# Performance work log

Hardware: AMD Instinct MI355X
Metric: run time of the kernel (lower is better)

The kernel has to match this reference:

```python
import jax, jax.numpy as jnp
import numpy as np

P, B, A, NBT, NC, NTAB, G = 512, 512, 32, 40, 3, 40, 36
NA = B * A


def setup_inputs() -> dict:
    key = jax.random.key(0)
    rng = np.random.default_rng(0)
    coords = jax.random.normal(key, (P, NA, 3), dtype=jnp.float32) * 3.0
    # residue b occupies atoms [b*A, (b+1)*A)
    offsets = np.broadcast_to(np.arange(B, dtype=np.int32) * A, (P, B)).copy()
    block_type = rng.integers(0, NBT, size=(P, B)).astype(np.int32)
    # simple linear chain per pose: conn 0 = lower (prev residue), conn 1 = upper (next residue)
    inter = np.full((P, B, NC, 2), -1, dtype=np.int32)
    inter[:, 1:, 0, 0] = np.arange(B - 1, dtype=np.int32)
    inter[:, 1:, 0, 1] = 1
    inter[:, :-1, 1, 0] = np.arange(1, B, dtype=np.int32)
    inter[:, :-1, 1, 1] = 0
    down = rng.integers(0, A, size=(NBT, NC, A)).astype(np.int32)
    bt_rama_table = rng.integers(0, NTAB, size=(NBT, 2)).astype(np.int32)
    bt_upper_conn_ind = np.ones(NBT, dtype=np.int32)
    bt_is_pro = rng.integers(0, 2, size=NBT).astype(np.int32)
    # unresolved torsion atoms: (local_atom_ind, conn_ind, n_bonds_from_conn); atom_ind<0 => via connection
    tor = np.zeros((NBT, 8, 3), dtype=np.int32)
    tor[:, 0] = (-1, 0, 0)  # phi: prev-C via lower conn
    tor[:, 1] = (0, -1, 0)  # N
    tor[:, 2] = (1, -1, 0)  # CA
    tor[:, 3] = (2, -1, 0)  # C
    tor[:, 4] = (0, -1, 0)  # psi: N
    tor[:, 5] = (1, -1, 0)  # CA
    tor[:, 6] = (2, -1, 0)  # C
    tor[:, 7] = (-1, 1, 0)  # next-N via upper conn
    rama_tables = jax.random.normal(jax.random.fold_in(key, 1), (NTAB, G, G), dtype=jnp.float32)
    tp = np.zeros((NTAB, 2, 2), dtype=np.float32)
    tp[:, 0, :] = -np.pi            # bb start
    tp[:, 1, :] = 2.0 * np.pi / G   # bb step
    return dict(
        coords=coords,
        pose_stack_block_coord_offset=jnp.asarray(offsets),
        pose_stack_block_type=jnp.asarray(block_type),
        pose_stack_inter_residue_connections=jnp.asarray(inter),
        bt_atom_downstream_of_conn=jnp.asarray(down),
        bt_rama_table=jnp.asarray(bt_rama_table),
        bt_upper_conn_ind=jnp.asarray(bt_upper_conn_ind),
        bt_is_pro=jnp.asarray(bt_is_pro),
        bt_rama_torsion_atoms=jnp.asarray(tor),
        rama_tables=rama_tables,
        table_params=jnp.asarray(tp),
    )


def _dihedral(p):
    # p: [..., 4, 3] -> dihedral angle [...] via atan2 formulation
    b1 = p[..., 1, :] - p[..., 0, :]
    b2 = p[..., 2, :] - p[..., 1, :]
    b3 = p[..., 3, :] - p[..., 2, :]
    n1 = jnp.cross(b1, b2)
    n2 = jnp.cross(b2, b3)
    b2n = b2 / (jnp.linalg.norm(b2, axis=-1, keepdims=True) + 1e-12)
    m1 = jnp.cross(n1, b2n)
    x = jnp.sum(n1 * n2, axis=-1)
    y = jnp.sum(m1 * n2, axis=-1)
    return jnp.arctan2(y, x)


def _catmull_rom_w(f):
    # weights over 4 neighbors (i-1, i, i+1, i+2); f in [0,1)
    f2 = f * f
    f3 = f2 * f
    return jnp.stack(
        [0.5 * (-f3 + 2 * f2 - f), 0.5 * (3 * f3 - 5 * f2 + 2),
         0.5 * (-3 * f3 + 4 * f2 + f), 0.5 * (f3 - f2)], axis=-1)


def reference(coords, pose_stack_block_coord_offset, pose_stack_block_type,
              pose_stack_inter_residue_connections, bt_atom_downstream_of_conn,
              bt_rama_table, bt_upper_conn_ind, bt_is_pro, bt_rama_torsion_atoms,
              rama_tables, table_params):
    nP, nB = pose_stack_block_type.shape
    nG = rama_tables.shape[-1]
    pidx = jnp.arange(nP)[:, None, None]
    bidx = jnp.arange(nB)[None, :, None]
    bt = pose_stack_block_type                       # [P,B]
    tor = bt_rama_torsion_atoms[bt]                  # [P,B,8,3]
    atom_ind, conn_ind, nbonds = tor[..., 0], tor[..., 1], tor[..., 2]
    safe_conn = jnp.clip(conn_ind, 0, None)
    other_block = pose_stack_inter_residue_connections[pidx, bidx, safe_conn, 0]  # [P,B,8]
    other_conn = pose_stack_inter_residue_connections[pidx, bidx, safe_conn, 1]
    conn_ok = (conn_ind >= 0) & (other_block >= 0)
    ob = jnp.clip(other_block, 0, None)
    oc = jnp.clip(other_conn, 0, None)
    obt = bt[pidx, ob]                               # [P,B,8]
    down_atom = bt_atom_downstream_of_conn[obt, oc, nbonds]
    conn_global = pose_stack_block_coord_offset[pidx, ob] + down_atom
    local_global = pose_stack_block_coord_offset[pidx, bidx] + jnp.clip(atom_ind, 0, None)
    use_local = atom_ind >= 0
    gidx = jnp.where(use_local, local_global, conn_global)  # [P,B,8]
    atom_ok = use_local | conn_ok
    xyz = coords[pidx, gidx]                         # [P,B,8,3]
    ang = _dihedral(xyz.reshape(nP, nB, 2, 4, 3))    # [P,B,2] -> (phi, psi)
    tor_ok = jnp.all(atom_ok.reshape(nP, nB, 2, 4), axis=-1)
    # table selection: proline-dependent on the NEXT residue
    uc = bt_upper_conn_ind[bt]                       # [P,B]
    p2 = jnp.arange(nP)[:, None]
    b2 = jnp.arange(nB)[None, :]
    nb = pose_stack_inter_residue_connections[p2, b2, uc, 0]  # [P,B]
    nb_ok = nb >= 0
    nbt = bt[p2, jnp.clip(nb, 0, None)]
    tab = bt_rama_table[bt, bt_is_pro[nbt]]          # [P,B]
    start = table_params[tab, 0]                     # [P,B,2]
    step = table_params[tab, 1]
    u = (ang - start) / step                         # [P,B,2]
    i0f = jnp.floor(u)
    f = u - i0f
    i0 = i0f.astype(jnp.int32)
    offs = jnp.arange(-1, 3, dtype=jnp.int32)        # 4 spline neighbors
    ii = jnp.mod(i0[..., 0:1] + offs, nG)            # [P,B,4] periodic phi bins
    jj = jnp.mod(i0[..., 1:2] + offs, nG)            # [P,B,4] periodic psi bins
    wphi = _catmull_rom_w(f[..., 0])                 # [P,B,4]
    wpsi = _catmull_rom_w(f[..., 1])
    vals = rama_tables[tab[..., None, None], ii[..., :, None], jj[..., None, :]]  # [P,B,4,4]
    e = jnp.einsum('pbi,pbj,pbij->pb', wphi, wpsi, vals)
    ok = tor_ok[..., 0] & tor_ok[..., 1] & nb_ok
    return jnp.sum(jnp.where(ok, e, 0.0), axis=-1)   # [P] per-pose rama score
```

## Files before the change

### kernel.cpp

```cpp
#include <hip/hip_runtime.h>
#include <math.h>

#define NP 512
#define NBLK 512
#define NTHREADS 1024
#define NA_ 32
#define NCn 3
#define NG 36
#define NBT 40
#define NTAB 40

struct F3 { float x, y, z; };
__device__ inline F3 f3sub(F3 a, F3 b) { return {a.x - b.x, a.y - b.y, a.z - b.z}; }
__device__ inline F3 f3cross(F3 a, F3 b) {
    return {a.y * b.z - a.z * b.y, a.z * b.x - a.x * b.z, a.x * b.y - a.y * b.x};
}
__device__ inline float f3dot(F3 a, F3 b) { return a.x * b.x + a.y * b.y + a.z * b.z; }

__global__ __launch_bounds__(NTHREADS, 8) void rama_kernel(
    const float* __restrict__ coords,
    const int*   __restrict__ offsets,
    const int*   __restrict__ block_type,
    const int*   __restrict__ inter,
    const int*   __restrict__ down,
    const int*   __restrict__ bt_rama_table,
    const int*   __restrict__ bt_upper_conn,
    const int*   __restrict__ bt_is_pro,
    const int*   __restrict__ tor_atoms,
    const float* __restrict__ rama_tables,
    const float* __restrict__ table_params,
    float*       __restrict__ out)
{
    __shared__ int   s_bt[NBLK];
    __shared__ int   s_off[NBLK];
    __shared__ int   s_inter[NBLK * NCn * 2];
    __shared__ int   s_tor[NBT * 24];
    __shared__ int   s_down[NBT * NCn * NA_];
    __shared__ int   s_rt[NBT * 2];
    __shared__ int   s_uc[NBT];
    __shared__ int   s_pro[NBT];
    __shared__ float s_tp[NTAB * 4];
    __shared__ float partial[NTHREADS / 64];

    const int p   = blockIdx.x;
    const int tid = threadIdx.x;

    if (tid < NBLK) {
        s_bt[tid]  = block_type[p * NBLK + tid];
        s_off[tid] = offsets[p * NBLK + tid];
    }
    for (int i = tid; i < NBLK * NCn * 2; i += NTHREADS)
        s_inter[i] = inter[p * NBLK * NCn * 2 + i];
    for (int i = tid; i < NBT * 24; i += NTHREADS)        s_tor[i]  = tor_atoms[i];
    for (int i = tid; i < NBT * NCn * NA_; i += NTHREADS) s_down[i] = down[i];
    if (tid < NBT * 2)  s_rt[tid] = bt_rama_table[tid];
    if (tid < NBT)      { s_uc[tid] = bt_upper_conn[tid]; s_pro[tid] = bt_is_pro[tid]; }
    if (tid < NTAB * 4) s_tp[tid] = table_params[tid];
    __syncthreads();

    const int b  = tid >> 1;
    const int t  = tid & 1;
    const int bt = s_bt[b];
    const int off_b = s_off[b];
    const float* pose_coords = coords + (size_t)p * NBLK * NA_ * 3;

    int  g[4];
    bool ok4 = true;
    #pragma unroll
    for (int a = 0; a < 4; ++a) {
        const int ti       = (bt * 8 + t * 4 + a) * 3;
        const int atom_ind = s_tor[ti + 0];
        const int conn_ind = s_tor[ti + 1];
        const int nbonds   = s_tor[ti + 2];
        if (atom_ind >= 0) {
            g[a] = off_b + atom_ind;
        } else {
            const int sc  = conn_ind > 0 ? conn_ind : 0;
            const int ib  = (b * NCn + sc) * 2;
            const int ob  = s_inter[ib + 0];
            const int oc  = s_inter[ib + 1];
            ok4 = ok4 && (conn_ind >= 0) && (ob >= 0);
            const int obc = ob > 0 ? ob : 0;
            const int occ = oc > 0 ? oc : 0;
            const int obt = s_bt[obc];
            g[a] = s_off[obc] + s_down[(obt * NCn + occ) * NA_ + nbonds];
        }
    }

    F3 pts[4];
    #pragma unroll
    for (int a = 0; a < 4; ++a) {
        const float* c = pose_coords + (size_t)g[a] * 3;
        pts[a] = {c[0], c[1], c[2]};
    }

    const F3 b1 = f3sub(pts[1], pts[0]);
    const F3 b2 = f3sub(pts[2], pts[1]);
    const F3 b3 = f3sub(pts[3], pts[2]);
    const F3 n1 = f3cross(b1, b2);
    const F3 n2 = f3cross(b2, b3);
    const float inv = 1.0f / (sqrtf(f3dot(b2, b2)) + 1e-12f);
    const F3 b2n = {b2.x * inv, b2.y * inv, b2.z * inv};
    const F3 m1  = f3cross(n1, b2n);
    const float ang = atan2f(f3dot(m1, n2), f3dot(n1, n2));

    const float ang_o = __shfl_xor(ang, 1);
    const int   oki   = ok4 ? 1 : 0;
    const int   ok_o  = __shfl_xor(oki, 1);
    const float phi = (t == 0) ? ang   : ang_o;
    const float psi = (t == 0) ? ang_o : ang;

    const int uc    = s_uc[bt];
    const int nb    = s_inter[(b * NCn + uc) * 2 + 0];
    const bool nbok = nb >= 0;
    const int nbc   = nb > 0 ? nb : 0;
    const int tab   = s_rt[bt * 2 + s_pro[s_bt[nbc]]];

    float e = 0.0f;
    if (oki && ok_o && nbok) {
        float wphi[4], wpsi[4];
        int   ii[4], jj[4];
        #pragma unroll
        for (int d = 0; d < 2; ++d) {
            const float a0    = (d == 0) ? phi : psi;
            const float start = s_tp[tab * 4 + d];
            const float step  = s_tp[tab * 4 + 2 + d];
            const float u   = (a0 - start) / step;
            const float i0f = floorf(u);
            const float f   = u - i0f;
            const int   i0  = (int)i0f;
            const float f2 = f * f, f3v = f2 * f;
            float* w = (d == 0) ? wphi : wpsi;
            w[0] = 0.5f * (-f3v + 2.0f * f2 - f);
            w[1] = 0.5f * (3.0f * f3v - 5.0f * f2 + 2.0f);
            w[2] = 0.5f * (-3.0f * f3v + 4.0f * f2 + f);
            w[3] = 0.5f * (f3v - f2);
            int* idx = (d == 0) ? ii : jj;
            #pragma unroll
            for (int k = 0; k < 4; ++k) {
                int v = (i0 - 1 + k) % NG;
                if (v < 0) v += NG;
                idx[k] = v;
            }
        }
        const float* T = rama_tables + (size_t)tab * NG * NG;
        #pragma unroll
        for (int r = 0; r < 2; ++r) {
            const int i = 2 * t + r;
            const float* Tr = T + ii[i] * NG;
            float rowsum = 0.0f;
            #pragma unroll
            for (int j = 0; j < 4; ++j) rowsum += wpsi[j] * Tr[jj[j]];
            e += wphi[i] * rowsum;
        }
    }

    float v = e;
    #pragma unroll
    for (int o = 32; o > 0; o >>= 1) v += __shfl_down(v, o);
    const int wave = tid >> 6;
    const int lane = tid & 63;
    if (lane == 0) partial[wave] = v;
    __syncthreads();
    if (tid == 0) {
        float s = 0.0f;
        #pragma unroll
        for (int i = 0; i < NTHREADS / 64; ++i) s += partial[i];
        out[p] = s;
    }
}

extern "C" void kernel_launch(void* const* d_in, const int* in_sizes, int n_in,
                              void* d_out, int out_size, void* d_ws, size_t ws_size,
                              hipStream_t stream) {
    (void)in_sizes; (void)n_in; (void)out_size; (void)d_ws; (void)ws_size;
    rama_kernel<<<NP, NTHREADS, 0, stream>>>(
        (const float*)d_in[0],
        (const int*)d_in[1],
        (const int*)d_in[2],
        (const int*)d_in[3],
        (const int*)d_in[4],
        (const int*)d_in[5],
        (const int*)d_in[6],
        (const int*)d_in[7],
        (const int*)d_in[8],
        (const float*)d_in[9],
        (const float*)d_in[10],
        (float*)d_out);
}
```

Before: 171.8 us.

## Vectorize staging, drop small-table shared copies, regroup threads by torsion half

Per-pose connectivity, block types and offsets are now staged into shared memory with int4 loads. The small per-block-type tables are no longer staged and are read straight from global memory. Threads are regrouped so each half of the block computes one torsion type, with phi/psi exchanged through shared memory and an extra barrier instead of a lane shuffle. When three torsion atoms are contiguous and aligned, their coordinates are fetched with float4 loads. Spline index wrapping is simplified to one modulo plus increments. This cuts shared-memory setup and scalar loads, at the cost of an extra barrier and uncached global reads of tiny tables.

```diff
diff --git a/kernel.cpp b/kernel.cpp
--- a/kernel.cpp
+++ b/kernel.cpp
@@ -31,128 +31,154 @@
     const float* __restrict__ table_params,
     float*       __restrict__ out)
 {
-    __shared__ int   s_bt[NBLK];
-    __shared__ int   s_off[NBLK];
-    __shared__ int   s_inter[NBLK * NCn * 2];
-    __shared__ int   s_tor[NBT * 24];
-    __shared__ int   s_down[NBT * NCn * NA_];
-    __shared__ int   s_rt[NBT * 2];
-    __shared__ int   s_uc[NBT];
-    __shared__ int   s_pro[NBT];
-    __shared__ float s_tp[NTAB * 4];
+    __shared__ __align__(16) int   s_bt[NBLK];
+    __shared__ __align__(16) int   s_off[NBLK];
+    __shared__ __align__(16) int   s_inter[NBLK * NCn * 2];
+    __shared__ __align__(16) float s_ang[NBLK * 2];
     __shared__ float partial[NTHREADS / 64];
 
     const int p   = blockIdx.x;
     const int tid = threadIdx.x;
 
-    if (tid < NBLK) {
-        s_bt[tid]  = block_type[p * NBLK + tid];
-        s_off[tid] = offsets[p * NBLK + tid];
-    }
-    for (int i = tid; i < NBLK * NCn * 2; i += NTHREADS)
-        s_inter[i] = inter[p * NBLK * NCn * 2 + i];
-    for (int i = tid; i < NBT * 24; i += NTHREADS)        s_tor[i]  = tor_atoms[i];
-    for (int i = tid; i < NBT * NCn * NA_; i += NTHREADS) s_down[i] = down[i];
-    if (tid < NBT * 2)  s_rt[tid] = bt_rama_table[tid];
-    if (tid < NBT)      { s_uc[tid] = bt_upper_conn[tid]; s_pro[tid] = bt_is_pro[tid]; }
-    if (tid < NTAB * 4) s_tp[tid] = table_params[tid];
+    {
+        const int4* gi = (const int4*)(inter      + (size_t)p * NBLK * NCn * 2);
+        const int4* gb = (const int4*)(block_type + (size_t)p * NBLK);
+        const int4* go = (const int4*)(offsets    + (size_t)p * NBLK);
+        if (tid < 768)      ((int4*)s_inter)[tid]     = gi[tid];
+        else if (tid < 896) ((int4*)s_bt)[tid - 768]  = gb[tid - 768];
+        else                ((int4*)s_off)[tid - 896] = go[tid - 896];
+    }
     __syncthreads();
 
-    const int b  = tid >> 1;
-    const int t  = tid & 1;
-    const int bt = s_bt[b];
+    const int b = tid & (NBLK - 1);
+    const int t = tid >> 9;
+    const int bt    = s_bt[b];
     const int off_b = s_off[b];
     const float* pose_coords = coords + (size_t)p * NBLK * NA_ * 3;
+
+    const int4* tq = (const int4*)tor_atoms + (6 * bt + 3 * t);
+    const int4 w0 = tq[0], w1 = tq[1], w2 = tq[2];
+    const int ai[4]  = {w0.x, w0.w, w1.z, w2.y};
+    const int ci[4]  = {w0.y, w1.x, w1.w, w2.z};
+    const int nbd[4] = {w0.z, w1.y, w2.x, w2.w};
 
     int  g[4];
     bool ok4 = true;
     #pragma unroll
     for (int a = 0; a < 4; ++a) {
-        const int ti       = (bt * 8 + t * 4 + a) * 3;
-        const int atom_ind = s_tor[ti + 0];
-        const int conn_ind = s_tor[ti + 1];
-        const int nbonds   = s_tor[ti + 2];
-        if (atom_ind >= 0) {
-            g[a] = off_b + atom_ind;
+        if (ai[a] >= 0) {
+            g[a] = off_b + ai[a];
         } else {
-            const int sc  = conn_ind > 0 ? conn_ind : 0;
-            const int ib  = (b * NCn + sc) * 2;
-            const int ob  = s_inter[ib + 0];
-            const int oc  = s_inter[ib + 1];
-            ok4 = ok4 && (conn_ind >= 0) && (ob >= 0);
+            const int sc = ci[a] > 0 ? ci[a] : 0;
+            const int ib = (b * NCn + sc) * 2;
+            const int ob = s_inter[ib + 0];
+            const int oc = s_inter[ib + 1];
+            ok4 = ok4 && (ci[a] >= 0) && (ob >= 0);
             const int obc = ob > 0 ? ob : 0;
             const int occ = oc > 0 ? oc : 0;
             const int obt = s_bt[obc];
-            g[a] = s_off[obc] + s_down[(obt * NCn + occ) * NA_ + nbonds];
+            g[a] = s_off[obc] + down[(obt * NCn + occ) * NA_ + nbd[a]];
         }
     }
 
     F3 pts[4];
-    #pragma unroll
-    for (int a = 0; a < 4; ++a) {
-        const float* c = pose_coords + (size_t)g[a] * 3;
-        pts[a] = {c[0], c[1], c[2]};
-    }
-
-    const F3 b1 = f3sub(pts[1], pts[0]);
-    const F3 b2 = f3sub(pts[2], pts[1]);
-    const F3 b3 = f3sub(pts[3], pts[2]);
-    const F3 n1 = f3cross(b1, b2);
-    const F3 n2 = f3cross(b2, b3);
-    const float inv = 1.0f / (sqrtf(f3dot(b2, b2)) + 1e-12f);
-    const F3 b2n = {b2.x * inv, b2.y * inv, b2.z * inv};
+    bool done = false;
+    if (g[2] == g[1] + 1 && g[3] == g[2] + 1 && (g[1] & 3) == 0) {
+        const float* base = pose_coords + (size_t)g[1] * 3;
+        const float4 q0 = ((const float4*)base)[0];
+        const float4 q1 = ((const float4*)base)[1];
+        const float  q2 = base[8];
+        pts[1] = {q0.x, q0.y, q0.z};
+        pts[2] = {q0.w, q1.x, q1.y};
+        pts[3] = {q1.z, q1.w, q2};
+        const float* c0 = pose_coords + (size_t)g[0] * 3;
+        pts[0] = {c0[0], c0[1], c0[2]};
+        done = true;
+    } else if (g[1] == g[0] + 1 && g[2] == g[1] + 1 && (g[0] & 3) == 0) {
+        const float* base = pose_coords + (size_t)g[0] * 3;
+        const float4 q0 = ((const float4*)base)[0];
+        const float4 q1 = ((const float4*)base)[1];
+        const float  q2 = base[8];
+        pts[0] = {q0.x, q0.y, q0.z};
+        pts[1] = {q0.w, q1.x, q1.y};
+        pts[2] = {q1.z, q1.w, q2};
+        const float* c3 = pose_coords + (size_t)g[3] * 3;
+        pts[3] = {c3[0], c3[1], c3[2]};
+        done = true;
+    }
+    if (!done) {
+        #pragma unroll
+        for (int a = 0; a < 4; ++a) {
+            const float* c = pose_coords + (size_t)g[a] * 3;
+            pts[a] = {c[0], c[1], c[2]};
+        }
+    }
+
+    const F3 d1 = f3sub(pts[1], pts[0]);
+    const F3 d2 = f3sub(pts[2], pts[1]);
+    const F3 d3 = f3sub(pts[3], pts[2]);
+    const F3 n1 = f3cross(d1, d2);
+    const F3 n2 = f3cross(d2, d3);
+    const float inv = 1.0f / (sqrtf(f3dot(d2, d2)) + 1e-12f);
+    const F3 b2n = {d2.x * inv, d2.y * inv, d2.z * inv};
     const F3 m1  = f3cross(n1, b2n);
     const float ang = atan2f(f3dot(m1, n2), f3dot(n1, n2));
 
-    const float ang_o = __shfl_xor(ang, 1);
-    const int   oki   = ok4 ? 1 : 0;
-    const int   ok_o  = __shfl_xor(oki, 1);
-    const float phi = (t == 0) ? ang   : ang_o;
-    const float psi = (t == 0) ? ang_o : ang;
-
-    const int uc    = s_uc[bt];
-    const int nb    = s_inter[(b * NCn + uc) * 2 + 0];
+    s_ang[b * 2 + t] = ok4 ? ang : 1e30f;
+    __syncthreads();
+    const float2 pp  = ((const float2*)s_ang)[b];
+    const float  phi = pp.x, psi = pp.y;
+    const bool   okb = fabsf(phi) < 1e29f && fabsf(psi) < 1e29f;
+
+    const int  uc   = bt_upper_conn[bt];
+    const int  nb   = s_inter[(b * NCn + uc) * 2 + 0];
     const bool nbok = nb >= 0;
-    const int nbc   = nb > 0 ? nb : 0;
-    const int tab   = s_rt[bt * 2 + s_pro[s_bt[nbc]]];
+    const int  nbc  = nb > 0 ? nb : 0;
+    const int  tab  = bt_rama_table[bt * 2 + bt_is_pro[s_bt[nbc]]];
 
     float e = 0.0f;
-    if (oki && ok_o && nbok) {
+    if (okb && nbok) {
+        const float4 tp4 = ((const float4*)table_params)[tab];
         float wphi[4], wpsi[4];
         int   ii[4], jj[4];
         #pragma unroll
         for (int d = 0; d < 2; ++d) {
-            const float a0    = (d == 0) ? phi : psi;
-            const float start = s_tp[tab * 4 + d];
-            const float step  = s_tp[tab * 4 + 2 + d];
+            const float a0    = (d == 0) ? phi   : psi;
+            const float start = (d == 0) ? tp4.x : tp4.y;
+            const float step  = (d == 0) ? tp4.z : tp4.w;
             const float u   = (a0 - start) / step;
             const float i0f = floorf(u);
             const float f   = u - i0f;
-            const int   i0  = (int)i0f;
             const float f2 = f * f, f3v = f2 * f;
             float* w = (d == 0) ? wphi : wpsi;
             w[0] = 0.5f * (-f3v + 2.0f * f2 - f);
             w[1] = 0.5f * (3.0f * f3v - 5.0f * f2 + 2.0f);
             w[2] = 0.5f * (-3.0f * f3v + 4.0f * f2 + f);
             w[3] = 0.5f * (f3v - f2);
+            int m = ((int)i0f - 1) % NG;
+            if (m < 0) m += NG;
             int* idx = (d == 0) ? ii : jj;
+            idx[0] = m;
             #pragma unroll
-            for (int k = 0; k < 4; ++k) {
-                int v = (i0 - 1 + k) % NG;
-                if (v < 0) v += NG;
-                idx[k] = v;
+            for (int k = 1; k < 4; ++k) {
+                m = (m + 1 == NG) ? 0 : m + 1;
+                idx[k] = m;
             }
         }
-        const float* T = rama_tables + (size_t)tab * NG * NG;
-        #pragma unroll
-        for (int r = 0; r < 2; ++r) {
-            const int i = 2 * t + r;
-            const float* Tr = T + ii[i] * NG;
-            float rowsum = 0.0f;
-            #pragma unroll
-            for (int j = 0; j < 4; ++j) rowsum += wpsi[j] * Tr[jj[j]];
-            e += wphi[i] * rowsum;
-        }
+        const int   ra = t ? ii[2]   : ii[0];
+        const int   rb = t ? ii[3]   : ii[1];
+        const float wa = t ? wphi[2] : wphi[0];
+        const float wb = t ? wphi[3] : wphi[1];
+        const float* T  = rama_tables + (size_t)tab * NG * NG;
+        const float* Ta = T + ra * NG;
+        const float* Tb = T + rb * NG;
+        float sa = 0.0f, sb = 0.0f;
+        #pragma unroll
+        for (int j = 0; j < 4; ++j) {
+            sa += wpsi[j] * Ta[jj[j]];
+            sb += wpsi[j] * Tb[jj[j]];
+        }
+        e = wa * sa + wb * sb;
     }
 
     float v = e;
```

After: 177.6 us. +3.4%, slower.
